# Performance work log

Hardware: AMD Instinct MI355X
Metric: run time of the kernel (lower is better)

The kernel has to match this reference:

```python
import jax, jax.numpy as jnp
import numpy as np

B, D, CIN, H, W = 2, 6, 3, 96, 96
DIM, NUM_HEADS, DEPTH = 144, 6, 2
WS = (2, 8, 8)   # window size (d, h, w)
SS = (1, 4, 4)   # shift size for odd blocks
HID = int(DIM * 2.0)
TBL = (2 * WS[0] - 1) * (2 * WS[1] - 1) * (2 * WS[2] - 1)  # 675
EPS = 1e-5


def _rpi(ws):
    # pairwise relative position index, same math as WindowAttention.get_position_index
    coords = np.stack(np.meshgrid(np.arange(ws[0]), np.arange(ws[1]), np.arange(ws[2]), indexing='ij'))
    cf = coords.reshape(3, -1).astype(np.int64)
    rc = (cf[:, :, None] - cf[:, None, :]).transpose(1, 2, 0)
    rc[..., 0] += ws[0] - 1
    rc[..., 1] += ws[1] - 1
    rc[..., 2] += ws[2] - 1
    rc[..., 0] *= (2 * ws[1] - 1) * (2 * ws[2] - 1)
    rc[..., 1] *= 2 * ws[2] - 1
    return rc.sum(-1)  # (N, N)


def _win_part_np(x, ws):
    b, d, h, w, c = x.shape
    x = x.reshape(b, d // ws[0], ws[0], h // ws[1], ws[1], w // ws[2], ws[2], c)
    return x.transpose(0, 1, 3, 5, 2, 4, 6, 7).reshape(-1, ws[0] * ws[1] * ws[2], c)


def _attn_mask(Dp, Hp, Wp, ws, ss):
    # static shift-window attention mask, same as compute_mask
    img = np.zeros((1, Dp, Hp, Wp, 1), np.float32)
    cnt = 0
    for d in (slice(-ws[0]), slice(-ws[0], -ss[0]), slice(-ss[0], None)):
        for h in (slice(-ws[1]), slice(-ws[1], -ss[1]), slice(-ss[1], None)):
            for w in (slice(-ws[2]), slice(-ws[2], -ss[2]), slice(-ss[2], None)):
                img[:, d, h, w, :] = cnt
                cnt += 1
    mw = _win_part_np(img, ws)[..., 0]  # (nW, N)
    am = mw[:, None, :] - mw[:, :, None]
    return np.where(am != 0, np.float32(-100.0), np.float32(0.0))


RPI = jnp.asarray(_rpi(WS))            # (N, N) int
MASK = jnp.asarray(_attn_mask(D, H, W, WS, SS))  # (nW, N, N)


def _ln(x, g, b):
    mu = jnp.mean(x, -1, keepdims=True)
    var = jnp.mean(jnp.square(x - mu), -1, keepdims=True)
    return (x - mu) * jax.lax.rsqrt(var + EPS) * g + b


def _win_part(x, ws):
    b, d, h, w, c = x.shape
    x = x.reshape(b, d // ws[0], ws[0], h // ws[1], ws[1], w // ws[2], ws[2], c)
    return x.transpose(0, 1, 3, 5, 2, 4, 6, 7).reshape(-1, ws[0] * ws[1] * ws[2], c)


def _win_rev(xw, ws, b, d, h, w):
    x = xw.reshape(b, d // ws[0], h // ws[1], w // ws[2], ws[0], ws[1], ws[2], -1)
    return x.transpose(0, 1, 4, 2, 5, 3, 6, 7).reshape(b, d, h, w, -1)


def _stl(x, i, shifted, params):
    # one Swin Transformer Layer; x: (B, D, H, W, C)
    n1g, n1b, qkvw, qkvb, rpb, projw, projb, n2g, n2b, fc1w, fc1b, fc2w, fc2b = params
    b, d, h, w, c = x.shape
    hd = c // NUM_HEADS
    scale = hd ** -0.5
    y = _ln(x, n1g[i], n1b[i])
    if shifted:
        y = jnp.roll(y, (-SS[0], -SS[1], -SS[2]), axis=(1, 2, 3))
    xw = _win_part(y, WS)  # (B_, N, C)
    B_, N, _ = xw.shape
    qkv = jnp.einsum('bnc,oc->bno', xw, qkvw[i]) + qkvb[i]
    qkv = qkv.reshape(B_, N, 3, NUM_HEADS, hd).transpose(2, 0, 3, 1, 4)
    q, k, v = qkv[0], qkv[1], qkv[2]
    attn = jnp.einsum('bhnd,bhmd->bhnm', q * scale, k)
    bias = rpb[i][RPI].transpose(2, 0, 1)  # (heads, N, N)
    attn = attn + bias[None]
    if shifted:
        nW = MASK.shape[0]
        attn = attn.reshape(B_ // nW, nW, NUM_HEADS, N, N) + MASK[None, :, None]
        attn = attn.reshape(B_, NUM_HEADS, N, N)
    attn = jax.nn.softmax(attn, axis=-1)
    out = jnp.einsum('bhnm,bhmd->bhnd', attn, v).transpose(0, 2, 1, 3).reshape(B_, N, c)
    out = jnp.einsum('bnc,oc->bno', out, projw[i]) + projb[i]
    y = _win_rev(out, WS, b, d, h, w)
    if shifted:
        y = jnp.roll(y, (SS[0], SS[1], SS[2]), axis=(1, 2, 3))
    x = x + y
    z = _ln(x, n2g[i], n2b[i])
    z = jnp.einsum('bdhwc,oc->bdhwo', z, fc1w[i]) + fc1b[i]
    z = jax.nn.gelu(z, approximate=False)
    z = jnp.einsum('bdhwo,co->bdhwc', z, fc2w[i]) + fc2b[i]
    return x + z


def setup_inputs() -> dict:
    key = jax.random.key(0)
    ks = jax.random.split(key, 8)
    s = 0.02
    return {
        'x': jax.random.normal(ks[0], (B, D, CIN, H, W), jnp.float32),
        'conv_w': jax.random.normal(ks[1], (DIM, CIN, 1, 3, 3), jnp.float32) * s,
        'conv_b': jnp.zeros((DIM,), jnp.float32),
        'ln0_g': jnp.ones((DIM,), jnp.float32),
        'ln0_b': jnp.zeros((DIM,), jnp.float32),
        'n1g': jnp.ones((DEPTH, DIM), jnp.float32),
        'n1b': jnp.zeros((DEPTH, DIM), jnp.float32),
        'qkvw': jax.random.normal(ks[2], (DEPTH, 3 * DIM, DIM), jnp.float32) * s,
        'qkvb': jnp.zeros((DEPTH, 3 * DIM), jnp.float32),
        'rpb': jax.random.normal(ks[3], (DEPTH, TBL, NUM_HEADS), jnp.float32) * s,
        'projw': jax.random.normal(ks[4], (DEPTH, DIM, DIM), jnp.float32) * s,
        'projb': jnp.zeros((DEPTH, DIM), jnp.float32),
        'n2g': jnp.ones((DEPTH, DIM), jnp.float32),
        'n2b': jnp.zeros((DEPTH, DIM), jnp.float32),
        'fc1w': jax.random.normal(ks[5], (DEPTH, HID, DIM), jnp.float32) * s,
        'fc1b': jnp.zeros((DEPTH, HID), jnp.float32),
        'fc2w': jax.random.normal(ks[6], (DEPTH, DIM, HID), jnp.float32) * s,
        'fc2b': jnp.zeros((DEPTH, DIM), jnp.float32),
        'lin_w': jax.random.normal(ks[7], (DIM, DIM), jnp.float32) * s,
        'lin_b': jnp.zeros((DIM,), jnp.float32),
        'ln1_g': jnp.ones((DIM,), jnp.float32),
        'ln1_b': jnp.zeros((DIM,), jnp.float32),
    }


def reference(x, conv_w, conv_b, ln0_g, ln0_b, n1g, n1b, qkvw, qkvb, rpb, projw, projb,
              n2g, n2b, fc1w, fc1b, fc2w, fc2b, lin_w, lin_b, ln1_g, ln1_b):
    # x: (n, d, c, h, w)
    y = x.transpose(0, 2, 1, 3, 4)  # n c d h w
    y = jax.lax.conv_general_dilated(
        y, conv_w, (1, 1, 1), [(0, 0), (1, 1), (1, 1)],
        dimension_numbers=('NCDHW', 'OIDHW', 'NCDHW')) + conv_b[None, :, None, None, None]
    y = y.transpose(0, 2, 3, 4, 1)  # n d h w c
    y = _ln(y, ln0_g, ln0_b)
    y = y.transpose(0, 4, 1, 2, 3)  # n c d h w
    params = (n1g, n1b, qkvw, qkvb, rpb, projw, projb, n2g, n2b, fc1w, fc1b, fc2w, fc2b)
    # RSTB (num_blocks = 1): residual group (STG of DEPTH STLs) + linear + skip
    f = y.transpose(0, 2, 3, 4, 1)  # b d h w c
    for i in range(DEPTH):
        f = _stl(f, i, i % 2 == 1, params)
    f = jnp.einsum('bdhwc,oc->bdhwo', f, lin_w) + lin_b
    y = y + f.transpose(0, 4, 1, 2, 3)
    # trailing LayerNorm and rearrange back to (n, d, c, h, w)
    out = _ln(y.transpose(0, 2, 3, 4, 1), ln1_g, ln1_b)
    return out.transpose(0, 1, 4, 2, 3)
```

## Files before the change

kernel.cpp:

```cpp
#include <hip/hip_runtime.h>
#include <math.h>

#define NTOK 110592
#define NWIN 864
#define TS   15925248

typedef unsigned short u16;
typedef unsigned int   u32;
typedef __attribute__((ext_vector_type(8))) short short8;
typedef __attribute__((ext_vector_type(4))) float float4v;

__device__ __forceinline__ float bf2f(u16 v) { return __uint_as_float(((u32)v) << 16); }
__device__ __forceinline__ u16 f2bf(float f) {
    u32 u = __float_as_uint(f);
    u32 r = u + 0x7fffu + ((u >> 16) & 1u);
    return (u16)(r >> 16);
}
__device__ __forceinline__ void unpack2(u32 u, float& lo, float& hi) {
    lo = __uint_as_float(u << 16);
    hi = __uint_as_float(u & 0xffff0000u);
}
__device__ __forceinline__ u32 pack2(float lo, float hi) {
    return (u32)f2bf(lo) | ((u32)f2bf(hi) << 16);
}
__device__ __forceinline__ float wave_sum(float v) {
    #pragma unroll
    for (int o = 32; o > 0; o >>= 1) v += __shfl_xor(v, o, 64);
    return v;
}

__device__ __forceinline__ void win_to_src(int tw, int shifted, int& sb, int& sd, int& sh, int& sw) {
    int n = tw & 127;
    int win = tw >> 7;
    int ww = win % 12;
    int wh = (win / 12) % 12;
    int rest = win / 144;
    int wd = rest % 3;
    sb = rest / 3;
    int ld = n >> 6, lh = (n >> 3) & 7, lw = n & 7;
    int dr = wd * 2 + ld, hr = wh * 8 + lh, wr = ww * 8 + lw;
    if (shifted) {
        sd = (dr + 1) % 6;
        sh = (hr + 4) % 96;
        sw = (wr + 4) % 96;
    } else {
        sd = dr; sh = hr; sw = wr;
    }
}

__global__ __launch_bounds__(256) void convert_weights(
    const float* __restrict__ qkvw, const float* __restrict__ projw,
    const float* __restrict__ fc1w, const float* __restrict__ fc2w,
    const float* __restrict__ linw, u16* __restrict__ wbuf,
    const float* __restrict__ rpb, float* __restrict__ bexp)
{
    int i = blockIdx.x * 256 + threadIdx.x;
    if (i < 124416) wbuf[i] = f2bf(qkvw[i]);
    else if (i < 165888) wbuf[i] = f2bf(projw[i - 124416]);
    else if (i < 248832) wbuf[i] = f2bf(fc1w[i - 165888]);
    else if (i < 331776) wbuf[i] = f2bf(fc2w[i - 248832]);
    else if (i < 352512) wbuf[i] = f2bf(linw[i - 331776]);
    else if (i < 549120) {
        int k = i - 352512;
        int n = k & 127, m = (k >> 7) & 127;
        int lh = k >> 14;
        int h = lh % 6, l = lh / 6;
        int rdi = (m >> 6) - (n >> 6) + 1;
        int rhi = ((m >> 3) & 7) - ((n >> 3) & 7) + 7;
        int rwi = (m & 7) - (n & 7) + 7;
        int bi = (rdi * 15 + rhi) * 15 + rwi;
        bexp[k] = rpb[l * 4050 + bi * 6 + h];
    }
}

__global__ __launch_bounds__(256) void conv_ln0_row(
    const float* __restrict__ x, const float* __restrict__ cw, const float* __restrict__ cb,
    const float* __restrict__ g0, const float* __restrict__ b0,
    float* __restrict__ y0)
{
    int bh = blockIdx.x;
    int h = bh % 96, bd = bh / 96;
    int b = bd / 6, d = bd - b * 6;
    __shared__ float ws[192][29];
    __shared__ float xsr[9][100];
    __shared__ float cbias[192], gg[144], bbv[144];
    int tid = threadIdx.x;

    for (int i = tid; i < 9 * 98; i += 256) {
        int row = i / 98, wx = i - row * 98;
        int ci = row / 3, kh = row - 3 * ci;
        int hh = h + kh - 1, wsrc = wx - 1;
        float v = 0.f;
        if (hh >= 0 && hh < 96 && wsrc >= 0 && wsrc < 96)
            v = x[((((size_t)b * 6 + d) * 3 + ci) * 96 + hh) * 96 + wsrc];
        xsr[row][wx] = v;
    }
    for (int i = tid; i < 192 * 27; i += 256) {
        int c = i / 27, j = i - c * 27;
        ws[c][j] = (c < 144) ? cw[c * 27 + j] : 0.f;
    }
    for (int i = tid; i < 192; i += 256) cbias[i] = (i < 144) ? cb[i] : 0.f;
    for (int i = tid; i < 144; i += 256) { gg[i] = g0[i]; bbv[i] = b0[i]; }
    __syncthreads();

    int wv = tid >> 6, lane = tid & 63;
    int p0 = wv * 24;

    float a0[24], a1[24], a2[24];
    #pragma unroll
    for (int k = 0; k < 24; k++) {
        a0[k] = cbias[lane]; a1[k] = cbias[lane + 64]; a2[k] = cbias[lane + 128];
    }

    for (int cikh = 0; cikh < 9; cikh++) {
        const float* xr = &xsr[cikh][p0];
        float xv[26];
        #pragma unroll
        for (int t = 0; t < 26; t++) xv[t] = xr[t];
        #pragma unroll
        for (int kw = 0; kw < 3; kw++) {
            int j = cikh * 3 + kw;
            float w0 = ws[lane][j], w1 = ws[lane + 64][j], w2 = ws[lane + 128][j];
            #pragma unroll
            for (int k = 0; k < 24; k++) {
                float xvv = xv[k + kw];
                a0[k] += w0 * xvv; a1[k] += w1 * xvv; a2[k] += w2 * xvv;
            }
        }
    }

    #pragma unroll
    for (int k = 0; k < 24; k++) {
        int p = p0 + k;
        float v0 = a0[k], v1 = a1[k];
        float v2m = (lane < 16) ? a2[k] : 0.f;
        float s  = wave_sum(v0 + v1 + v2m);
        float s2 = wave_sum(v0 * v0 + v1 * v1 + v2m * v2m);
        float mu = s * (1.f / 144.f);
        float rstd = rsqrtf(fmaxf(s2 * (1.f / 144.f) - mu * mu, 0.f) + 1e-5f);
        size_t o = ((size_t)bh * 96 + p) * 144;
        float r0 = (v0 - mu) * rstd * gg[lane] + bbv[lane];
        float r1 = (v1 - mu) * rstd * gg[lane + 64] + bbv[lane + 64];
        y0[o + lane] = r0;
        y0[o + lane + 64] = r1;
        if (lane < 16) {
            float r2 = (a2[k] - mu) * rstd * gg[lane + 128] + bbv[lane + 128];
            y0[o + lane + 128] = r2;
        }
    }
}

template<int MODE>
__global__ __launch_bounds__(256) void ln_gather(
    const float* __restrict__ in, u16* __restrict__ out,
    const float* __restrict__ g, const float* __restrict__ bt)
{
    int tok = blockIdx.x * 4 + (threadIdx.x >> 6);
    int lane = threadIdx.x & 63;
    int src;
    if (MODE == 0) src = tok;
    else {
        int b, d, h, w;
        win_to_src(tok, MODE == 2, b, d, h, w);
        src = ((b * 6 + d) * 96 + h) * 96 + w;
    }
    const float* row = in + (size_t)src * 144;
    float v0 = row[lane], v1 = row[lane + 64], v2 = (lane < 16) ? row[lane + 128] : 0.f;
    float s  = wave_sum(v0 + v1 + v2);
    float s2 = wave_sum(v0 * v0 + v1 * v1 + v2 * v2);
    float mu = s * (1.f / 144.f);
    float rstd = rsqrtf(fmaxf(s2 * (1.f / 144.f) - mu * mu, 0.f) + 1e-5f);
    u16* orow = out + (size_t)tok * 144;
    orow[lane]      = f2bf((v0 - mu) * rstd * g[lane]      + bt[lane]);
    orow[lane + 64] = f2bf((v1 - mu) * rstd * g[lane + 64] + bt[lane + 64]);
    if (lane < 16)
        orow[lane + 128] = f2bf((v2 - mu) * rstd * g[lane + 128] + bt[lane + 128]);
}

template<int AMODE, int EPI, int SHIFTED, int ADDBIAS, int KTILES>
__global__ __launch_bounds__(192) void mgemm(
    const void* __restrict__ Asrc, const u16* __restrict__ Wt, const float* __restrict__ bias,
    u16* __restrict__ outb, float* __restrict__ fres, const float* __restrict__ y0,
    int a_add, int a_ld, int w_ld, int o_ld, int o_add)
{
    __shared__ u16 As[64 * 152];
    int m0 = blockIdx.y * 64, n0 = blockIdx.x * 144;
    int tid = threadIdx.x;
    int wv3 = tid / 64, lane = tid & 63;
    int mrow = lane & 15, quad = lane >> 4;
    const short8 z8 = {0, 0, 0, 0, 0, 0, 0, 0};

    float4v acc[4][3];
    #pragma unroll
    for (int i = 0; i < 4; i++)
        #pragma unroll
        for (int j = 0; j < 3; j++) acc[i][j] = (float4v){0.f, 0.f, 0.f, 0.f};

    #pragma unroll
    for (int kt = 0; kt < KTILES; kt++) {
        if (kt) __syncthreads();
        if (AMODE == 2) {
            const u16* A = (const u16*)Asrc;
            #pragma unroll
            for (int idx = tid; idx < 1152; idx += 192) {
                int r = idx / 18, c4 = idx - r * 18;
                *(short8*)&As[r * 152 + c4 * 8] =
                    *(const short8*)&A[(size_t)(a_add + m0 + r) * a_ld + kt * 144 + c4 * 8];
            }
        } else {
            const float* A = (const float*)Asrc;
            #pragma unroll
            for (int idx = tid; idx < 2304; idx += 192) {
                int r = idx / 36, c4 = idx - r * 36;
                const float4* src4 = (const float4*)&A[(size_t)(a_add + m0 + r) * a_ld + kt * 144];
                float4 v = src4[c4];
                *(u32*)&As[r * 152 + c4 * 4]     = pack2(v.x, v.y);
                *(u32*)&As[r * 152 + c4 * 4 + 2] = pack2(v.z, v.w);
            }
        }
        __syncthreads();

        const u16* Wg = Wt + (size_t)(n0 + wv3 * 48 + mrow) * w_ld + kt * 144;

        #pragma unroll
        for (int ks = 0; ks < 4; ks++) {
            int k0 = ks * 32;
            short8 af[4], bf[3];
            #pragma unroll
            for (int i = 0; i < 4; i++)
                af[i] = *(const short8*)&As[(i * 16 + mrow) * 152 + k0 + quad * 8];
            #pragma unroll
            for (int j = 0; j < 3; j++)
                bf[j] = *(const short8*)&Wg[(size_t)j * 16 * w_ld + k0 + quad * 8];
            #pragma unroll
            for (int i = 0; i < 4; i++)
                #pragma unroll
                for (int j = 0; j < 3; j++)
                    acc[i][j] = __builtin_amdgcn_mfma_f32_16x16x32_bf16(af[i], bf[j], acc[i][j], 0, 0, 0);
        }
        {
            bool tl = (quad < 2);
            short8 af[4], bf[3];
            #pragma unroll
            for (int i = 0; i < 4; i++)
                af[i] = tl ? *(const short8*)&As[(i * 16 + mrow) * 152 + 128 + quad * 8] : z8;
            #pragma unroll
            for (int j = 0; j < 3; j++)
                bf[j] = tl ? *(const short8*)&Wg[(size_t)j * 16 * w_ld + 128 + quad * 8] : z8;
            #pragma unroll
            for (int i = 0; i < 4; i++)
                #pragma unroll
                for (int j = 0; j < 3; j++)
                    acc[i][j] = __builtin_amdgcn_mfma_f32_16x16x32_bf16(af[i], bf[j], acc[i][j], 0, 0, 0);
        }
    }

    #pragma unroll
    for (int i = 0; i < 4; i++) {
        #pragma unroll
        for (int reg = 0; reg < 4; reg++) {
            int m = m0 + i * 16 + quad * 4 + reg;
            int orow;
            if (EPI == 2 || EPI == 5) {
                int b, d, h, w;
                win_to_src(m, SHIFTED, b, d, h, w);
                orow = ((b * 6 + d) * 96 + h) * 96 + w;
            } else orow = m + o_add;
            #pragma unroll
            for (int j = 0; j < 3; j++) {
                int n = n0 + wv3 * 48 + j * 16 + mrow;
                float v = acc[i][j][reg];
                if (ADDBIAS) v += bias[n];
                if (EPI == 1) v = 0.5f * v * (1.f + erff(v * 0.70710678118f));
                if (EPI == 2 || EPI == 3) {
                    fres[(size_t)orow * 144 + n] += v;
                } else if (EPI == 5) {
                    fres[(size_t)orow * 144 + n] = y0[(size_t)orow * 144 + n] + v;
                } else {
                    if (EPI == 4) v += y0[(size_t)orow * o_ld + n];
                    if (EPI == 6 && n < 144) v *= 0.20412414523193154f;
                    outb[(size_t)orow * o_ld + n] = f2bf(v);
                }
            }
        }
    }
}

template<int SHIFTED>
__global__ __launch_bounds__(256) void attn_mfma(
    const u16* __restrict__ qkv,
    const float* __restrict__ bexp,
    u16* __restrict__ tok_out, int win_base)
{
    int win = blockIdx.x;
    int head = blockIdx.y;
    __shared__ __align__(16) u16 Pb[4][32][136];
    __shared__ __align__(16) u16 Vt[24][136];
    __shared__ float invden_s[128];
    __shared__ unsigned char reg_s[128];

    int tid = threadIdx.x;
    int wv = tid >> 6, lane = tid & 63;
    int c = lane & 15, quad = lane >> 4;
    int qbase = wv * 32;
    const short8 z8 = {0, 0, 0, 0, 0, 0, 0, 0};
    const float* bh_ = bexp + head * 16384;

    if (tid < 128) {
        const u32* vsrc = (const u32*)(qkv + ((size_t)win * 128 + tid) * 432) + 144 + head * 12;
        #pragma unroll
        for (int i = 0; i < 12; i++) {
            u32 u = vsrc[i];
            Vt[2 * i][tid]     = (u16)(u & 0xffffu);
            Vt[2 * i + 1][tid] = (u16)(u >> 16);
        }
    }
    if (SHIFTED && tid < 128) {
        int t = tid;
        int gwin = win_base + win;
        int wib = gwin % 432;
        int wwn = wib % 12, whn = (wib / 12) % 12, wdn = wib / 144;
        int ld = t >> 6, lh = (t >> 3) & 7, lw = t & 7;
        int dr = wdn * 2 + ld, hr = whn * 8 + lh, wr = wwn * 8 + lw;
        int rd = (dr < 4) ? 0 : ((dr < 5) ? 1 : 2);
        int rh = (hr < 88) ? 0 : ((hr < 92) ? 1 : 2);
        int rw = (wr < 88) ? 0 : ((wr < 92) ? 1 : 2);
        reg_s[t] = (unsigned char)(rd * 9 + rh * 3 + rw);
    }
    __syncthreads();

    short8 aq[2];
    #pragma unroll
    for (int i = 0; i < 2; i++) {
        aq[i] = z8;
        if (quad < 3)
            aq[i] = *(const short8*)(qkv + ((size_t)win * 128 + qbase + i * 16 + c) * 432
                                     + head * 24 + quad * 8);
    }

    float4v s_acc[2][8];
    #pragma unroll
    for (int i = 0; i < 2; i++)
        #pragma unroll
        for (int j = 0; j < 8; j++) s_acc[i][j] = (float4v){0.f, 0.f, 0.f, 0.f};

    #pragma unroll
    for (int j = 0; j < 8; j++) {
        short8 kf = z8;
        if (quad < 3)
            kf = *(const short8*)(qkv + ((size_t)win * 128 + j * 16 + c) * 432
                                  + 144 + head * 24 + quad * 8);
        s_acc[0][j] = __builtin_amdgcn_mfma_f32_16x16x32_bf16(aq[0], kf, s_acc[0][j], 0, 0, 0);
        s_acc[1][j] = __builtin_amdgcn_mfma_f32_16x16x32_bf16(aq[1], kf, s_acc[1][j], 0, 0, 0);
    }

    int kreg[8];
    #pragma unroll
    for (int j = 0; j < 8; j++)
        kreg[j] = SHIFTED ? (int)reg_s[j * 16 + c] : 0;
    #pragma unroll
    for (int i = 0; i < 2; i++) {
        #pragma unroll
        for (int r = 0; r < 4; r++) {
            int ml = i * 16 + quad * 4 + r;
            int m = qbase + ml;
            const float* brow = bh_ + m * 128;
            int myreg = SHIFTED ? (int)reg_s[m] : 0;
            float sv[8];
            float vmax = -1e30f;
            #pragma unroll
            for (int j = 0; j < 8; j++) {
                float s = s_acc[i][j][r] + brow[j * 16 + c];
                if (SHIFTED && kreg[j] != myreg) s -= 100.f;
                sv[j] = s;
                vmax = fmaxf(vmax, s);
            }
            #pragma unroll
            for (int o = 8; o >= 1; o >>= 1) vmax = fmaxf(vmax, __shfl_xor(vmax, o, 64));
            float den = 0.f;
            #pragma unroll
            for (int j = 0; j < 8; j++) {
                float p = __expf(sv[j] - vmax);
                den += p;
                Pb[wv][ml][j * 16 + c] = f2bf(p);
            }
            #pragma unroll
            for (int o = 8; o >= 1; o >>= 1) den += __shfl_xor(den, o, 64);
            if (c == 0) invden_s[m] = 1.f / den;
        }
    }

    float4v o_acc[2][2];
    #pragma unroll
    for (int i = 0; i < 2; i++)
        #pragma unroll
        for (int jv = 0; jv < 2; jv++) o_acc[i][jv] = (float4v){0.f, 0.f, 0.f, 0.f};

    #pragma unroll
    for (int ks = 0; ks < 4; ks++) {
        short8 pf0 = *(const short8*)&Pb[wv][c][ks * 32 + quad * 8];
        short8 pf1 = *(const short8*)&Pb[wv][16 + c][ks * 32 + quad * 8];
        short8 vf0 = *(const short8*)&Vt[c][ks * 32 + quad * 8];
        short8 vf1 = (c < 8) ? *(const short8*)&Vt[16 + c][ks * 32 + quad * 8] : z8;
        o_acc[0][0] = __builtin_amdgcn_mfma_f32_16x16x32_bf16(pf0, vf0, o_acc[0][0], 0, 0, 0);
        o_acc[0][1] = __builtin_amdgcn_mfma_f32_16x16x32_bf16(pf0, vf1, o_acc[0][1], 0, 0, 0);
        o_acc[1][0] = __builtin_amdgcn_mfma_f32_16x16x32_bf16(pf1, vf0, o_acc[1][0], 0, 0, 0);
        o_acc[1][1] = __builtin_amdgcn_mfma_f32_16x16x32_bf16(pf1, vf1, o_acc[1][1], 0, 0, 0);
    }

    float* ob = (float*)&Pb[wv][0][0];
    #pragma unroll
    for (int i = 0; i < 2; i++)
        #pragma unroll
        for (int jv = 0; jv < 2; jv++) {
            int d = jv * 16 + c;
            if (d < 24) {
                #pragma unroll
                for (int r = 0; r < 4; r++)
                    ob[(i * 16 + quad * 4 + r) * 26 + d] = o_acc[i][jv][r];
            }
        }
    __syncthreads();

    if (tid < 128) {
        const float2* ol = (const float2*)((const float*)&Pb[0][0][0]
                                           + (tid >> 5) * 2176 + (tid & 31) * 26);
        float inv = invden_s[tid];
        u32* orow = (u32*)tok_out + ((size_t)((win_base + win) * 128 + tid)) * 72 + head * 12;
        #pragma unroll
        for (int d2 = 0; d2 < 12; d2++) {
            float2 v = ol[d2];
            orow[d2] = pack2(v.x * inv, v.y * inv);
        }
    }
}

__global__ __launch_bounds__(256) void final_ln_out_kernel(
    const u16* __restrict__ gsrc, const float* __restrict__ g, const float* __restrict__ bt,
    float* __restrict__ out)
{
    int bh = blockIdx.x;
    int h = bh % 96, d = (bh / 96) % 6, b = bh / 576;
    __shared__ u16 tile[96][152];
    __shared__ float stat[96][2];
    const u16* src = gsrc + (size_t)bh * 96 * 144;
    for (int i = threadIdx.x; i < 1728; i += 256) {
        int wt = i / 18, c8 = i - wt * 18;
        *(short8*)&tile[wt][c8 * 8] = *(const short8*)&src[wt * 144 + c8 * 8];
    }
    __syncthreads();
    if (threadIdx.x < 96) {
        const u32* row = (const u32*)&tile[threadIdx.x][0];
        float s = 0.f, s2 = 0.f;
        #pragma unroll
        for (int j = 0; j < 72; j++) {
            float lo, hi; unpack2(row[j], lo, hi);
            s += lo + hi; s2 += lo * lo + hi * hi;
        }
        float mu = s * (1.f / 144.f);
        float var = s2 * (1.f / 144.f) - mu * mu;
        stat[threadIdx.x][0] = mu;
        stat[threadIdx.x][1] = rsqrtf(fmaxf(var, 0.f) + 1e-5f);
    }
    __syncthreads();
    size_t obase = ((size_t)(b * 6 + d) * 144) * 9216 + h * 96;
    for (int i = threadIdx.x; i < 96 * 144; i += blockDim.x) {
        int c = i / 96, wt = i - c * 96;
        out[obase + (size_t)c * 9216 + wt] =
            (bf2f(tile[wt][c]) - stat[wt][0]) * stat[wt][1] * g[c] + bt[c];
    }
}

extern "C" void kernel_launch(void* const* d_in, const int* in_sizes, int n_in,
                              void* d_out, int out_size, void* d_ws, size_t ws_size,
                              hipStream_t stream) {
    const float* x     = (const float*)d_in[0];
    const float* convw = (const float*)d_in[1];
    const float* convb = (const float*)d_in[2];
    const float* ln0g  = (const float*)d_in[3];
    const float* ln0b  = (const float*)d_in[4];
    const float* n1g   = (const float*)d_in[5];
    const float* n1b   = (const float*)d_in[6];
    const float* qkvw  = (const float*)d_in[7];
    const float* qkvb  = (const float*)d_in[8];
    const float* rpb   = (const float*)d_in[9];
    const float* projw = (const float*)d_in[10];
    const float* projb = (const float*)d_in[11];
    const float* n2g   = (const float*)d_in[12];
    const float* n2b   = (const float*)d_in[13];
    const float* fc1w  = (const float*)d_in[14];
    const float* fc1b  = (const float*)d_in[15];
    const float* fc2w  = (const float*)d_in[16];
    const float* fc2b  = (const float*)d_in[17];
    const float* linw  = (const float*)d_in[18];
    const float* linb  = (const float*)d_in[19];
    const float* ln1g  = (const float*)d_in[20];
    const float* ln1b  = (const float*)d_in[21];

    char* wp = (char*)d_ws;
    float* f    = (float*)wp;             wp += (size_t)TS * 4;
    u16*   tok  = (u16*)wp;               wp += (size_t)TS * 2;
    u16*   wbuf = (u16*)wp;               wp += 352512ull * 2;
    float* bexp = (float*)wp;             wp += 196608ull * 4;
    u16*   qkvbuf = (u16*)wp;
    size_t rest = ws_size - (size_t)(wp - (char*)d_ws);
    int nch = (rest >= (size_t)NTOK * 432 * 2) ? 1
            : (rest >= (size_t)NTOK * 216 * 2) ? 2 : 4;
    int nm  = (rest >= (size_t)NTOK * 288 * 2) ? 1
            : (rest >= (size_t)NTOK * 144 * 2) ? 2 : 3;
    float* y0 = (float*)d_out;

    convert_weights<<<2145, 256, 0, stream>>>(qkvw, projw, fc1w, fc2w, linw, wbuf, rpb, bexp);
    conv_ln0_row<<<1152, 256, 0, stream>>>(x, convw, convb, ln0g, ln0b, y0);

    for (int layer = 0; layer < 2; ++layer) {
        const u16* qw  = wbuf + (size_t)layer * 62208;
        const u16* pw  = wbuf + 124416 + (size_t)layer * 20736;
        const u16* f1w = wbuf + 165888 + (size_t)layer * 41472;
        const u16* f2w = wbuf + 248832 + (size_t)layer * 41472;
        const float* qb  = qkvb + (size_t)layer * 432;
        const float* pb  = projb + (size_t)layer * 144;
        const float* g1  = n1g + layer * 144;
        const float* b1  = n1b + layer * 144;
        const float* g2  = n2g + layer * 144;
        const float* b2  = n2b + layer * 144;
        const float* f1b = fc1b + (size_t)layer * 288;
        const float* f2b = fc2b + (size_t)layer * 144;
        const float* bx  = bexp + (size_t)layer * 98304;

        if (layer == 0) ln_gather<1><<<NTOK / 4, 256, 0, stream>>>(y0, tok, g1, b1);
        else            ln_gather<2><<<NTOK / 4, 256, 0, stream>>>(f, tok, g1, b1);

        int chtok = NTOK / nch, chwin = NWIN / nch;
        for (int c = 0; c < nch; c++) {
            mgemm<2, 6, 0, 1, 1><<<dim3(3, chtok / 64), 192, 0, stream>>>(
                tok, qw, qb, qkvbuf, nullptr, nullptr,
                c * chtok, 144, 144, 432, 0);
            if (layer == 0)
                attn_mfma<0><<<dim3(chwin, 6), 256, 0, stream>>>(qkvbuf, bx, tok, c * chwin);
            else
                attn_mfma<1><<<dim3(chwin, 6), 256, 0, stream>>>(qkvbuf, bx, tok, c * chwin);
        }

        if (layer == 0)
            mgemm<2, 5, 0, 1, 1><<<dim3(1, NTOK / 64), 192, 0, stream>>>(
                tok, pw, pb, nullptr, f, y0, 0, 144, 144, 144, 0);
        else
            mgemm<2, 2, 1, 1, 1><<<dim3(1, NTOK / 64), 192, 0, stream>>>(
                tok, pw, pb, nullptr, f, nullptr, 0, 144, 144, 144, 0);

        ln_gather<0><<<NTOK / 4, 256, 0, stream>>>(f, tok, g2, b2);

        int fcch = NTOK / nm;
        for (int c = 0; c < nm; c++) {
            int mst = c * fcch;
            mgemm<2, 1, 0, 1, 1><<<dim3(2, fcch / 64), 192, 0, stream>>>(
                tok, f1w, f1b, qkvbuf, nullptr, nullptr, mst, 144, 144, 288, 0);
            mgemm<2, 3, 0, 1, 2><<<dim3(1, fcch / 64), 192, 0, stream>>>(
                qkvbuf, f2w, f2b, nullptr, f, nullptr, 0, 288, 288, 144, mst);
        }
    }

    mgemm<0, 4, 0, 1, 1><<<dim3(1, NTOK / 64), 192, 0, stream>>>(
        f, wbuf + 331776, linb, tok, nullptr, y0, 0, 144, 144, 144, 0);

    final_ln_out_kernel<<<2 * 6 * 96, 256, 0, stream>>>(tok, ln1g, ln1b, (float*)d_out);
}
```

Baseline: 852.0 us.

## Store QKV head-major and interleave softmax with PV per row block in attention

The QKV GEMM epilogue now writes its output in a head-major layout (head, token, 72 = q|k|v of 24 each), so each attention block reads one contiguous 144-byte row per token instead of strided slices from a 432-wide row. The attention kernel also runs the P·V MFMAs right after each 16-row softmax chunk, which halves the shared-memory P buffer and may improve occupancy and overlap. The cost is scattered bf16 stores in the GEMM epilogue, since consecutive n values now map to different head planes.

```diff
diff --git a/kernel.cpp b/kernel.cpp
--- a/kernel.cpp
+++ b/kernel.cpp
@@ -276,9 +276,14 @@
                     fres[(size_t)orow * 144 + n] += v;
                 } else if (EPI == 5) {
                     fres[(size_t)orow * 144 + n] = y0[(size_t)orow * 144 + n] + v;
+                } else if (EPI == 6) {
+                    int slot = n / 144;
+                    int hn = n - slot * 144;
+                    int head = hn / 24, dd = hn - head * 24;
+                    if (slot == 0) v *= 0.20412414523193154f;
+                    outb[((size_t)head * o_ld + orow) * 72 + slot * 24 + dd] = f2bf(v);
                 } else {
                     if (EPI == 4) v += y0[(size_t)orow * o_ld + n];
-                    if (EPI == 6 && n < 144) v *= 0.20412414523193154f;
                     outb[(size_t)orow * o_ld + n] = f2bf(v);
                 }
             }
@@ -290,11 +295,11 @@
 __global__ __launch_bounds__(256) void attn_mfma(
     const u16* __restrict__ qkv,
     const float* __restrict__ bexp,
-    u16* __restrict__ tok_out, int win_base)
+    u16* __restrict__ tok_out, int win_base, int chtok)
 {
     int win = blockIdx.x;
     int head = blockIdx.y;
-    __shared__ __align__(16) u16 Pb[4][32][136];
+    __shared__ __align__(16) u16 Pb[4][16][136];
     __shared__ __align__(16) u16 Vt[24][136];
     __shared__ float invden_s[128];
     __shared__ unsigned char reg_s[128];
@@ -305,9 +310,10 @@
     int qbase = wv * 32;
     const short8 z8 = {0, 0, 0, 0, 0, 0, 0, 0};
     const float* bh_ = bexp + head * 16384;
+    const u16* base = qkv + ((size_t)head * chtok + (size_t)win * 128) * 72;
 
     if (tid < 128) {
-        const u32* vsrc = (const u32*)(qkv + ((size_t)win * 128 + tid) * 432) + 144 + head * 12;
+        const u32* vsrc = (const u32*)(base + (size_t)tid * 72 + 48);
         #pragma unroll
         for (int i = 0; i < 12; i++) {
             u32 u = vsrc[i];
@@ -334,8 +340,7 @@
     for (int i = 0; i < 2; i++) {
         aq[i] = z8;
         if (quad < 3)
-            aq[i] = *(const short8*)(qkv + ((size_t)win * 128 + qbase + i * 16 + c) * 432
-                                     + head * 24 + quad * 8);
+            aq[i] = *(const short8*)(base + (size_t)(qbase + i * 16 + c) * 72 + quad * 8);
     }
 
     float4v s_acc[2][8];
@@ -348,8 +353,7 @@
     for (int j = 0; j < 8; j++) {
         short8 kf = z8;
         if (quad < 3)
-            kf = *(const short8*)(qkv + ((size_t)win * 128 + j * 16 + c) * 432
-                                  + 144 + head * 24 + quad * 8);
+            kf = *(const short8*)(base + (size_t)(j * 16 + c) * 72 + 24 + quad * 8);
         s_acc[0][j] = __builtin_amdgcn_mfma_f32_16x16x32_bf16(aq[0], kf, s_acc[0][j], 0, 0, 0);
         s_acc[1][j] = __builtin_amdgcn_mfma_f32_16x16x32_bf16(aq[1], kf, s_acc[1][j], 0, 0, 0);
     }
@@ -358,12 +362,19 @@
     #pragma unroll
     for (int j = 0; j < 8; j++)
         kreg[j] = SHIFTED ? (int)reg_s[j * 16 + c] : 0;
+
+    float4v o_acc[2][2];
+    #pragma unroll
+    for (int i = 0; i < 2; i++)
+        #pragma unroll
+        for (int jv = 0; jv < 2; jv++) o_acc[i][jv] = (float4v){0.f, 0.f, 0.f, 0.f};
+
     #pragma unroll
     for (int i = 0; i < 2; i++) {
         #pragma unroll
         for (int r = 0; r < 4; r++) {
-            int ml = i * 16 + quad * 4 + r;
-            int m = qbase + ml;
+            int ml = quad * 4 + r;
+            int m = qbase + i * 16 + ml;
             const float* brow = bh_ + m * 128;
             int myreg = SHIFTED ? (int)reg_s[m] : 0;
             float sv[8];
@@ -388,24 +399,14 @@
             for (int o = 8; o >= 1; o >>= 1) den += __shfl_xor(den, o, 64);
             if (c == 0) invden_s[m] = 1.f / den;
         }
-    }
-
-    float4v o_acc[2][2];
-    #pragma unroll
-    for (int i = 0; i < 2; i++)
-        #pragma unroll
-        for (int jv = 0; jv < 2; jv++) o_acc[i][jv] = (float4v){0.f, 0.f, 0.f, 0.f};
-
-    #pragma unroll
-    for (int ks = 0; ks < 4; ks++) {
-        short8 pf0 = *(const short8*)&Pb[wv][c][ks * 32 + quad * 8];
-        short8 pf1 = *(const short8*)&Pb[wv][16 + c][ks * 32 + quad * 8];
-        short8 vf0 = *(const short8*)&Vt[c][ks * 32 + quad * 8];
-        short8 vf1 = (c < 8) ? *(const short8*)&Vt[16 + c][ks * 32 + quad * 8] : z8;
-        o_acc[0][0] = __builtin_amdgcn_mfma_f32_16x16x32_bf16(pf0, vf0, o_acc[0][0], 0, 0, 0);
-        o_acc[0][1] = __builtin_amdgcn_mfma_f32_16x16x32_bf16(pf0, vf1, o_acc[0][1], 0, 0, 0);
-        o_acc[1][0] = __builtin_amdgcn_mfma_f32_16x16x32_bf16(pf1, vf0, o_acc[1][0], 0, 0, 0);
-        o_acc[1][1] = __builtin_amdgcn_mfma_f32_16x16x32_bf16(pf1, vf1, o_acc[1][1], 0, 0, 0);
+        #pragma unroll
+        for (int ks = 0; ks < 4; ks++) {
+            short8 pf  = *(const short8*)&Pb[wv][c][ks * 32 + quad * 8];
+            short8 vf0 = *(const short8*)&Vt[c][ks * 32 + quad * 8];
+            short8 vf1 = (c < 8) ? *(const short8*)&Vt[16 + c][ks * 32 + quad * 8] : z8;
+            o_acc[i][0] = __builtin_amdgcn_mfma_f32_16x16x32_bf16(pf, vf0, o_acc[i][0], 0, 0, 0);
+            o_acc[i][1] = __builtin_amdgcn_mfma_f32_16x16x32_bf16(pf, vf1, o_acc[i][1], 0, 0, 0);
+        }
     }
 
     float* ob = (float*)&Pb[wv][0][0];
@@ -424,7 +425,7 @@
 
     if (tid < 128) {
         const float2* ol = (const float2*)((const float*)&Pb[0][0][0]
-                                           + (tid >> 5) * 2176 + (tid & 31) * 26);
+                                           + (tid >> 5) * 1088 + (tid & 31) * 26);
         float inv = invden_s[tid];
         u32* orow = (u32*)tok_out + ((size_t)((win_base + win) * 128 + tid)) * 72 + head * 12;
         #pragma unroll
@@ -535,11 +536,11 @@
         for (int c = 0; c < nch; c++) {
             mgemm<2, 6, 0, 1, 1><<<dim3(3, chtok / 64), 192, 0, stream>>>(
                 tok, qw, qb, qkvbuf, nullptr, nullptr,
-                c * chtok, 144, 144, 432, 0);
+                c * chtok, 144, 144, chtok, 0);
             if (layer == 0)
-                attn_mfma<0><<<dim3(chwin, 6), 256, 0, stream>>>(qkvbuf, bx, tok, c * chwin);
+                attn_mfma<0><<<dim3(chwin, 6), 256, 0, stream>>>(qkvbuf, bx, tok, c * chwin, chtok);
             else
-                attn_mfma<1><<<dim3(chwin, 6), 256, 0, stream>>>(qkvbuf, bx, tok, c * chwin);
+                attn_mfma<1><<<dim3(chwin, 6), 256, 0, stream>>>(qkvbuf, bx, tok, c * chwin, chtok);
         }
 
         if (layer == 0)
```

Result: faster. 835.2 us (-2.0%).
